# Performance work log

Hardware: AMD Instinct MI355X
Metric: run time of the kernel (lower is better)

## Reference

```python
import jax, jax.numpy as jnp
import numpy as np

B_, C_, H_, W_ = 4, 512, 64, 64

def setup_inputs() -> dict:
    key = jax.random.key(0)
    kx, kb, kc, kd, kg = jax.random.split(key, 5)
    scale = 1.0 / np.sqrt(C_)
    x = jax.random.normal(kx, (B_, C_, H_, W_), dtype=jnp.float32)
    Wb = jax.random.normal(kb, (C_, C_), dtype=jnp.float32) * scale
    Wc = jax.random.normal(kc, (C_, C_), dtype=jnp.float32) * scale
    Wd = jax.random.normal(kd, (C_, C_), dtype=jnp.float32) * scale
    gamma = jax.random.normal(kg, (1,), dtype=jnp.float32) * 0.1
    return {"x": x, "Wb": Wb, "Wc": Wc, "Wd": Wd, "gamma": gamma}

def reference(x, Wb, Wc, Wd, gamma):
    b, c, h, w = x.shape
    n = h * w
    xf = x.reshape(b, c, n)                       # (b, c, N)
    # 1x1 convs (bias=False) == per-pixel channel matmuls
    Bm = jnp.einsum('oc,bcn->bon', Wb, xf)        # (b, c, N)
    Cm = jnp.einsum('oc,bcn->bon', Wc, xf)
    Dm = jnp.einsum('oc,bcn->bon', Wd, xf)
    # S = softmax(B^T C, axis=2): (b, N, N), no scaling (faithful to source)
    S = jax.nn.softmax(jnp.einsum('bcn,bcm->bnm', Bm, Cm), axis=-1)
    # attention_maps = D @ S^T : (b, c, N)
    att = jnp.einsum('bcm,bnm->bcn', Dm, S).reshape(b, c, h, w)
    return gamma * att + x
```

## Files before the change

### kernel.cpp

```cpp
#include <hip/hip_runtime.h>
#include <math.h>
#include <stdint.h>

#define CC 512
#define NN 4096
#define BB 4

typedef _Float16 f16;
typedef _Float16 f16x8 __attribute__((ext_vector_type(8)));
typedef _Float16 f16x4 __attribute__((ext_vector_type(4)));
typedef float f32x4 __attribute__((ext_vector_type(4)));

__device__ __forceinline__ void gload_lds16(const void* g, void* l) {
    __builtin_amdgcn_global_load_lds(
        (const __attribute__((address_space(1))) void*)g,
        (__attribute__((address_space(3))) void*)l, 16, 0, 0);
}

template<int ROWS>
__device__ __forceinline__ void stage_tile(const f16* __restrict__ g, int stride_e,
                                           f16* lds, int wid, int lane) {
    constexpr int ITERS = ROWS * 8 / 64 / 4;
    #pragma unroll
    for (int it = 0; it < ITERS; ++it) {
        int flatbase = (wid * ITERS + it) * 64;
        f16* dst = lds + flatbase * 8;
        int flat = flatbase + lane;
        int r = flat >> 3, c = flat & 7;
        const f16* src = g + (size_t)r * stride_e + ((c ^ (r & 7)) << 3);
        gload_lds16(src, dst);
    }
}

__device__ __forceinline__ f16x8 frag_ld(const f16* lds, int r, int ch) {
    return *(const f16x8*)(lds + r * 64 + ((ch ^ (r & 7)) << 3));
}

#define MFMA16(a, b, c) __builtin_amdgcn_mfma_f32_16x16x32_f16((a), (b), (c), 0, 0, 0)

__device__ __forceinline__ f32x4 redmax16(f32x4 v) {
    #pragma unroll
    for (int off = 1; off < 16; off <<= 1) {
        f32x4 o;
        #pragma unroll
        for (int q = 0; q < 4; ++q) o[q] = __shfl_xor(v[q], off);
        #pragma unroll
        for (int q = 0; q < 4; ++q) v[q] = fmaxf(v[q], o[q]);
    }
    return v;
}
__device__ __forceinline__ f32x4 redsum16(f32x4 v) {
    #pragma unroll
    for (int off = 1; off < 16; off <<= 1) {
        f32x4 o;
        #pragma unroll
        for (int q = 0; q < 4; ++q) o[q] = __shfl_xor(v[q], off);
        #pragma unroll
        for (int q = 0; q < 4; ++q) v[q] += o[q];
    }
    return v;
}

__global__ __launch_bounds__(256) void wcvt_k(const float* __restrict__ Wb,
                                              const float* __restrict__ Wc,
                                              const float* __restrict__ Wd,
                                              f16* __restrict__ W16) {
    int i = blockIdx.x * 256 + threadIdx.x;
    int idx = i * 4;
    int m = idx >> 18;
    int off = idx & 262143;
    const float* src = (m == 0) ? Wb : (m == 1) ? Wc : Wd;
    f32x4 v = *(const f32x4*)(src + off);
    f16x4 h = { (f16)v[0], (f16)v[1], (f16)v[2], (f16)v[3] };
    *(f16x4*)(W16 + idx) = h;
}

__global__ __launch_bounds__(256) void proj_k(const float* __restrict__ x,
                                              const f16* __restrict__ W16,
                                              f16* __restrict__ Bt, f16* __restrict__ Ct,
                                              f16* __restrict__ Dm) {
    const int wsel = blockIdx.z % 3;
    const int b = blockIdx.z / 3;
    const f16* __restrict__ W = W16 + (size_t)wsel * CC * CC;
    const float* __restrict__ X = x + (size_t)b * CC * NN;
    const size_t p16 = (size_t)CC * NN;
    const int o0 = blockIdx.y * 128, n0 = blockIdx.x * 128;

    __shared__ __align__(16) char smraw[34816];
    f16* As = (f16*)smraw;
    f16* Bs = As + 128 * 64;
    f16* T  = (f16*)smraw;

    const int t = threadIdx.x;
    const int wid = t >> 6, lane = t & 63;
    const int wr = wid >> 1, wc = wid & 1;

    f32x4 acc[4][4] = {};
    const int cg = t & 7;
    const int n4 = ((t >> 3) & 31) * 4;

    for (int kc = 0; kc < CC; kc += 64) {
        __syncthreads();
        stage_tile<128>(W + (size_t)o0 * CC + kc, CC, As, wid, lane);
        f32x4 v[8];
        #pragma unroll
        for (int i = 0; i < 8; ++i)
            v[i] = *(const f32x4*)(X + (size_t)(kc + cg * 8 + i) * NN + n0 + n4);
        #pragma unroll
        for (int j = 0; j < 4; ++j) {
            f16x8 h = { (f16)v[0][j], (f16)v[1][j], (f16)v[2][j], (f16)v[3][j],
                        (f16)v[4][j], (f16)v[5][j], (f16)v[6][j], (f16)v[7][j] };
            int r = n4 + j;
            *(f16x8*)(Bs + r * 64 + ((cg ^ (r & 7)) << 3)) = h;
        }
        __syncthreads();
        #pragma unroll
        for (int ks = 0; ks < 2; ++ks) {
            int ch = ks * 4 + (lane >> 4);
            f16x8 a[4], bb[4];
            #pragma unroll
            for (int i = 0; i < 4; ++i) a[i]  = frag_ld(As, wr * 64 + i * 16 + (lane & 15), ch);
            #pragma unroll
            for (int j = 0; j < 4; ++j) bb[j] = frag_ld(Bs, wc * 64 + j * 16 + (lane & 15), ch);
            #pragma unroll
            for (int i = 0; i < 4; ++i)
                #pragma unroll
                for (int j = 0; j < 4; ++j)
                    acc[i][j] = MFMA16(a[i], bb[j], acc[i][j]);
        }
    }

    __syncthreads();
    if (wsel < 2) {
        #pragma unroll
        for (int i = 0; i < 4; ++i)
            #pragma unroll
            for (int j = 0; j < 4; ++j) {
                int n_l = wc * 64 + j * 16 + (lane & 15);
                int o_l = wr * 64 + i * 16 + (lane >> 4) * 4;
                f16x4 h = { (f16)acc[i][j][0], (f16)acc[i][j][1], (f16)acc[i][j][2], (f16)acc[i][j][3] };
                *(f16x4*)(T + n_l * 136 + o_l) = h;
            }
        __syncthreads();
        f16* __restrict__ dst = ((wsel == 0) ? Bt : Ct) + (size_t)b * p16;
        int n = t & 127;
        #pragma unroll
        for (int it = 0; it < 8; ++it) {
            int ch8 = (t >> 7) * 8 + it;
            f16x8 h = *(f16x8*)(T + n * 136 + ch8 * 8);
            *(f16x8*)(dst + (size_t)(n0 + n) * CC + o0 + ch8 * 8) = h;
        }
    } else {
        #pragma unroll
        for (int i = 0; i < 4; ++i)
            #pragma unroll
            for (int j = 0; j < 4; ++j) {
                int n_l = wc * 64 + j * 16 + (lane & 15);
                #pragma unroll
                for (int q = 0; q < 4; ++q) {
                    int o_l = wr * 64 + i * 16 + (lane >> 4) * 4 + q;
                    T[o_l * 136 + n_l] = (f16)acc[i][j][q];
                }
            }
        __syncthreads();
        f16* __restrict__ dst = Dm + (size_t)b * p16;
        int o = t & 127;
        #pragma unroll
        for (int it = 0; it < 8; ++it) {
            int ch8 = (t >> 7) * 8 + it;
            f16x8 h = *(f16x8*)(T + o * 136 + ch8 * 8);
            *(f16x8*)(dst + (size_t)(o0 + o) * NN + n0 + ch8 * 8) = h;
        }
    }
}

__global__ __launch_bounds__(512, 2) void flash_k(
    const float* __restrict__ x, const float* __restrict__ gamma_p,
    const f16* __restrict__ Bt, const f16* __restrict__ Ct,
    const f16* __restrict__ Dm, float* __restrict__ out)
{
    __shared__ __align__(16) char sm[140288];
    f16* CtS = (f16*)sm;
    f16* DtS = (f16*)(sm + 65536);
    f16* PS  = (f16*)(sm + 131072);
    float* mxp = (float*)(sm + 139264);
    float* lp  = (float*)(sm + 139776);

    const int bx = blockIdx.x;
    const int j8 = bx & 7;
    const int b = j8 >> 1;
    const int n0 = ((bx >> 3) + (j8 & 1) * 32) * 64;

    const size_t p16 = (size_t)CC * NN;
    const f16* __restrict__ Btb = Bt + (size_t)b * p16;
    const f16* __restrict__ Ctb = Ct + (size_t)b * p16;
    const f16* __restrict__ Dmb = Dm + (size_t)b * p16;

    const int t = threadIdx.x;
    const int wid = t >> 6, lane = t & 63;
    const int wr = wid >> 1, w1 = wid & 1;
    const int l15 = lane & 15, g = lane >> 4;

    f16x8 Q[16];
    {
        const f16* qrow = Btb + (size_t)(n0 + wr * 16 + l15) * CC + g * 8;
        #pragma unroll
        for (int s = 0; s < 16; ++s) Q[s] = *(const f16x8*)(qrow + s * 32);
    }

    f32x4 O[16];
    #pragma unroll
    for (int i = 0; i < 16; ++i) O[i] = (f32x4)(0.f);
    f32x4 m_run = (f32x4)(-INFINITY);
    f32x4 l_run = (f32x4)(0.f);

    for (int m0 = 0; m0 < NN; m0 += 64) {
        __syncthreads();
        #pragma unroll
        for (int it = 0; it < 8; ++it) {
            int r = wid * 8 + it;
            f16* dst = CtS + r * 512;
            const f16* src = Ctb + (size_t)(m0 + r) * CC + ((lane ^ (r & 7)) << 3);
            gload_lds16(src, dst);
        }
        #pragma unroll
        for (int it = 0; it < 8; ++it) {
            int flatbase = (wid * 8 + it) * 64;
            f16* dst = DtS + flatbase * 8;
            int flat = flatbase + lane;
            int r = flat >> 3, c = flat & 7;
            const f16* src = Dmb + (size_t)r * NN + m0 + ((c ^ (r & 7)) << 3);
            gload_lds16(src, dst);
        }
        __syncthreads();

        f32x4 S0 = (f32x4)(0.f), S1 = (f32x4)(0.f);
        #pragma unroll
        for (int s = 0; s < 16; ++s) {
            int ch = s * 4 + g;
            int mr0 = w1 * 32 + l15;
            int mr1 = mr0 + 16;
            f16x8 b0 = *(const f16x8*)(CtS + mr0 * 512 + (((ch ^ (mr0 & 7)) & 63) << 3));
            f16x8 b1 = *(const f16x8*)(CtS + mr1 * 512 + (((ch ^ (mr1 & 7)) & 63) << 3));
            S0 = MFMA16(Q[s], b0, S0);
            S1 = MFMA16(Q[s], b1, S1);
        }
        f32x4 tm;
        #pragma unroll
        for (int q = 0; q < 4; ++q) tm[q] = fmaxf(S0[q], S1[q]);
        tm = redmax16(tm);
        if (l15 == 0) *(f32x4*)(mxp + w1 * 64 + wr * 16 + g * 4) = tm;
        __syncthreads();
        f32x4 t0 = *(const f32x4*)(mxp + wr * 16 + g * 4);
        f32x4 t1 = *(const f32x4*)(mxp + 64 + wr * 16 + g * 4);
        f32x4 mnew, scl, p0, p1, ps;
        #pragma unroll
        for (int q = 0; q < 4; ++q) {
            mnew[q] = fmaxf(m_run[q], fmaxf(t0[q], t1[q]));
            scl[q] = __expf(m_run[q] - mnew[q]);
            p0[q] = __expf(S0[q] - mnew[q]);
            p1[q] = __expf(S1[q] - mnew[q]);
            ps[q] = p0[q] + p1[q];
        }
        m_run = mnew;
        ps = redsum16(ps);
        if (l15 == 0) *(f32x4*)(lp + w1 * 64 + wr * 16 + g * 4) = ps;
        #pragma unroll
        for (int q = 0; q < 4; ++q) {
            int row = wr * 16 + g * 4 + q;
            int c0 = w1 * 32 + l15;
            int c1 = c0 + 16;
            PS[row * 64 + ((((c0 >> 3) ^ (row & 7)) << 3) | (c0 & 7))] = (f16)p0[q];
            PS[row * 64 + ((((c1 >> 3) ^ (row & 7)) << 3) | (c1 & 7))] = (f16)p1[q];
        }
        __syncthreads();
        f32x4 lp0 = *(const f32x4*)(lp + wr * 16 + g * 4);
        f32x4 lp1 = *(const f32x4*)(lp + 64 + wr * 16 + g * 4);
        #pragma unroll
        for (int q = 0; q < 4; ++q) l_run[q] = l_run[q] * scl[q] + lp0[q] + lp1[q];
        #pragma unroll
        for (int i = 0; i < 16; ++i)
            #pragma unroll
            for (int q = 0; q < 4; ++q) O[i][q] *= scl[q];
        int prow = wr * 16 + l15;
        f16x8 pa0 = *(const f16x8*)(PS + prow * 64 + (((g ^ (prow & 7)) & 7) << 3));
        f16x8 pa1 = *(const f16x8*)(PS + prow * 64 + ((((4 + g) ^ (prow & 7)) & 7) << 3));
        #pragma unroll
        for (int jj = 0; jj < 16; ++jj) {
            int crow = w1 * 256 + jj * 16 + l15;
            f16x8 d0 = *(const f16x8*)(DtS + crow * 64 + (((g ^ (crow & 7)) & 7) << 3));
            f16x8 d1 = *(const f16x8*)(DtS + crow * 64 + ((((4 + g) ^ (crow & 7)) & 7) << 3));
            O[jj] = MFMA16(pa0, d0, O[jj]);
            O[jj] = MFMA16(pa1, d1, O[jj]);
        }
    }

    __syncthreads();
    const float gam = gamma_p[0];
    f32x4 inv;
    #pragma unroll
    for (int q = 0; q < 4; ++q) inv[q] = gam / l_run[q];
    float* T = (float*)sm;
    #pragma unroll
    for (int jj = 0; jj < 16; ++jj) {
        int crow = w1 * 256 + jj * 16 + l15;
        f32x4 v;
        #pragma unroll
        for (int q = 0; q < 4; ++q) v[q] = O[jj][q] * inv[q];
        *(f32x4*)(T + crow * 68 + wr * 16 + g * 4) = v;
    }
    __syncthreads();
    const float* __restrict__ xb = x + (size_t)b * CC * NN;
    float* __restrict__ ob = out + (size_t)b * CC * NN;
    #pragma unroll
    for (int it = 0; it < 16; ++it) {
        int c = (t >> 4) + it * 32;
        int n4 = (t & 15) * 4;
        f32x4 v = *(const f32x4*)(T + c * 68 + n4);
        f32x4 xv = *(const f32x4*)(xb + (size_t)c * NN + n0 + n4);
        #pragma unroll
        for (int q = 0; q < 4; ++q) v[q] += xv[q];
        *(f32x4*)(ob + (size_t)c * NN + n0 + n4) = v;
    }
}

extern "C" void kernel_launch(void* const* d_in, const int* in_sizes, int n_in,
                              void* d_out, int out_size, void* d_ws, size_t ws_size,
                              hipStream_t stream) {
    const float* x  = (const float*)d_in[0];
    const float* Wb = (const float*)d_in[1];
    const float* Wc = (const float*)d_in[2];
    const float* Wd = (const float*)d_in[3];
    const float* gm = (const float*)d_in[4];
    float* out = (float*)d_out;
    char* ws = (char*)d_ws;

    f16* W16 = (f16*)(ws);
    f16* Bt  = (f16*)(ws + 1572864);
    f16* Ct  = (f16*)(ws + 1572864 + 16777216);
    f16* Dm  = (f16*)(ws + 1572864 + 2 * 16777216);

    wcvt_k<<<dim3(768), 256, 0, stream>>>(Wb, Wc, Wd, W16);
    proj_k<<<dim3(32, 4, 12), 256, 0, stream>>>(x, W16, Bt, Ct, Dm);
    flash_k<<<dim3(256), 512, 0, stream>>>(x, gm, Bt, Ct, Dm, out);
}
```

Baseline: 385.5 us.

## Remap waves to 2x4 grid so each wave reuses LDS fragments across two row tiles

The eight waves move from a 4x2 layout (16 query rows, 32 keys, 256 output channels each) to a 2x4 layout (32 query rows, 16 keys, 128 output channels each). Each C and D fragment read from LDS now feeds two MFMAs, one per query row tile, which roughly halves LDS read traffic per MFMA in both the QK^T and PV phases. The cost is more Q registers per wave (32 fragments instead of 16), a cross-wave max/sum reduction over four partials instead of two, and a larger LDS footprint. s_setprio hints are also placed around the MFMA loops.

```diff
diff --git a/kernel.cpp b/kernel.cpp
--- a/kernel.cpp
+++ b/kernel.cpp
@@ -179,12 +179,12 @@
     const f16* __restrict__ Bt, const f16* __restrict__ Ct,
     const f16* __restrict__ Dm, float* __restrict__ out)
 {
-    __shared__ __align__(16) char sm[140288];
+    __shared__ __align__(16) char sm[141312];
     f16* CtS = (f16*)sm;
     f16* DtS = (f16*)(sm + 65536);
     f16* PS  = (f16*)(sm + 131072);
     float* mxp = (float*)(sm + 139264);
-    float* lp  = (float*)(sm + 139776);
+    float* lp  = (float*)(sm + 140288);
 
     const int bx = blockIdx.x;
     const int j8 = bx & 7;
@@ -198,21 +198,25 @@
 
     const int t = threadIdx.x;
     const int wid = t >> 6, lane = t & 63;
-    const int wr = wid >> 1, w1 = wid & 1;
+    const int a = wid >> 2, mj = wid & 3;
     const int l15 = lane & 15, g = lane >> 4;
-
-    f16x8 Q[16];
-    {
-        const f16* qrow = Btb + (size_t)(n0 + wr * 16 + l15) * CC + g * 8;
-        #pragma unroll
-        for (int s = 0; s < 16; ++s) Q[s] = *(const f16x8*)(qrow + s * 32);
-    }
-
-    f32x4 O[16];
-    #pragma unroll
-    for (int i = 0; i < 16; ++i) O[i] = (f32x4)(0.f);
-    f32x4 m_run = (f32x4)(-INFINITY);
-    f32x4 l_run = (f32x4)(0.f);
+    const int nb = a * 32 + g * 4;
+
+    f16x8 Q[2][16];
+    #pragma unroll
+    for (int f = 0; f < 2; ++f) {
+        const f16* qrow = Btb + (size_t)(n0 + a * 32 + f * 16 + l15) * CC + g * 8;
+        #pragma unroll
+        for (int s = 0; s < 16; ++s) Q[f][s] = *(const f16x8*)(qrow + s * 32);
+    }
+
+    f32x4 O[2][8];
+    #pragma unroll
+    for (int f = 0; f < 2; ++f)
+        #pragma unroll
+        for (int j = 0; j < 8; ++j) O[f][j] = (f32x4)(0.f);
+    f32x4 m_run[2] = { (f32x4)(-INFINITY), (f32x4)(-INFINITY) };
+    f32x4 l_run[2] = { (f32x4)(0.f), (f32x4)(0.f) };
 
     for (int m0 = 0; m0 < NN; m0 += 64) {
         __syncthreads();
@@ -235,80 +239,115 @@
         __syncthreads();
 
         f32x4 S0 = (f32x4)(0.f), S1 = (f32x4)(0.f);
+        const int mr = mj * 16 + l15;
+        __builtin_amdgcn_s_setprio(1);
         #pragma unroll
         for (int s = 0; s < 16; ++s) {
-            int ch = s * 4 + g;
-            int mr0 = w1 * 32 + l15;
-            int mr1 = mr0 + 16;
-            f16x8 b0 = *(const f16x8*)(CtS + mr0 * 512 + (((ch ^ (mr0 & 7)) & 63) << 3));
-            f16x8 b1 = *(const f16x8*)(CtS + mr1 * 512 + (((ch ^ (mr1 & 7)) & 63) << 3));
-            S0 = MFMA16(Q[s], b0, S0);
-            S1 = MFMA16(Q[s], b1, S1);
-        }
-        f32x4 tm;
-        #pragma unroll
-        for (int q = 0; q < 4; ++q) tm[q] = fmaxf(S0[q], S1[q]);
-        tm = redmax16(tm);
-        if (l15 == 0) *(f32x4*)(mxp + w1 * 64 + wr * 16 + g * 4) = tm;
-        __syncthreads();
-        f32x4 t0 = *(const f32x4*)(mxp + wr * 16 + g * 4);
-        f32x4 t1 = *(const f32x4*)(mxp + 64 + wr * 16 + g * 4);
-        f32x4 mnew, scl, p0, p1, ps;
+            f16x8 bfrag = *(const f16x8*)(CtS + mr * 512 + ((((s * 4 + g) ^ (mr & 7)) & 63) << 3));
+            S0 = MFMA16(Q[0][s], bfrag, S0);
+            S1 = MFMA16(Q[1][s], bfrag, S1);
+        }
+        __builtin_amdgcn_s_setprio(0);
+        f32x4 tm0 = redmax16(S0);
+        f32x4 tm1 = redmax16(S1);
+        if (l15 == 0) {
+            *(f32x4*)(mxp + mj * 64 + nb) = tm0;
+            *(f32x4*)(mxp + mj * 64 + nb + 16) = tm1;
+        }
+        __syncthreads();
+        f32x4 mnew[2], scl[2], p0, p1;
+        #pragma unroll
+        for (int f = 0; f < 2; ++f) {
+            f32x4 c0 = *(const f32x4*)(mxp + 0 * 64 + nb + f * 16);
+            f32x4 c1 = *(const f32x4*)(mxp + 1 * 64 + nb + f * 16);
+            f32x4 c2 = *(const f32x4*)(mxp + 2 * 64 + nb + f * 16);
+            f32x4 c3 = *(const f32x4*)(mxp + 3 * 64 + nb + f * 16);
+            #pragma unroll
+            for (int q = 0; q < 4; ++q) {
+                mnew[f][q] = fmaxf(m_run[f][q],
+                                   fmaxf(fmaxf(c0[q], c1[q]), fmaxf(c2[q], c3[q])));
+                scl[f][q] = __expf(m_run[f][q] - mnew[f][q]);
+            }
+            m_run[f] = mnew[f];
+        }
         #pragma unroll
         for (int q = 0; q < 4; ++q) {
-            mnew[q] = fmaxf(m_run[q], fmaxf(t0[q], t1[q]));
-            scl[q] = __expf(m_run[q] - mnew[q]);
-            p0[q] = __expf(S0[q] - mnew[q]);
-            p1[q] = __expf(S1[q] - mnew[q]);
-            ps[q] = p0[q] + p1[q];
-        }
-        m_run = mnew;
-        ps = redsum16(ps);
-        if (l15 == 0) *(f32x4*)(lp + w1 * 64 + wr * 16 + g * 4) = ps;
-        #pragma unroll
-        for (int q = 0; q < 4; ++q) {
-            int row = wr * 16 + g * 4 + q;
-            int c0 = w1 * 32 + l15;
-            int c1 = c0 + 16;
-            PS[row * 64 + ((((c0 >> 3) ^ (row & 7)) << 3) | (c0 & 7))] = (f16)p0[q];
-            PS[row * 64 + ((((c1 >> 3) ^ (row & 7)) << 3) | (c1 & 7))] = (f16)p1[q];
-        }
-        __syncthreads();
-        f32x4 lp0 = *(const f32x4*)(lp + wr * 16 + g * 4);
-        f32x4 lp1 = *(const f32x4*)(lp + 64 + wr * 16 + g * 4);
-        #pragma unroll
-        for (int q = 0; q < 4; ++q) l_run[q] = l_run[q] * scl[q] + lp0[q] + lp1[q];
-        #pragma unroll
-        for (int i = 0; i < 16; ++i)
-            #pragma unroll
-            for (int q = 0; q < 4; ++q) O[i][q] *= scl[q];
-        int prow = wr * 16 + l15;
-        f16x8 pa0 = *(const f16x8*)(PS + prow * 64 + (((g ^ (prow & 7)) & 7) << 3));
-        f16x8 pa1 = *(const f16x8*)(PS + prow * 64 + ((((4 + g) ^ (prow & 7)) & 7) << 3));
-        #pragma unroll
-        for (int jj = 0; jj < 16; ++jj) {
-            int crow = w1 * 256 + jj * 16 + l15;
-            f16x8 d0 = *(const f16x8*)(DtS + crow * 64 + (((g ^ (crow & 7)) & 7) << 3));
-            f16x8 d1 = *(const f16x8*)(DtS + crow * 64 + ((((4 + g) ^ (crow & 7)) & 7) << 3));
-            O[jj] = MFMA16(pa0, d0, O[jj]);
-            O[jj] = MFMA16(pa1, d1, O[jj]);
+            p0[q] = __expf(S0[q] - mnew[0][q]);
+            p1[q] = __expf(S1[q] - mnew[1][q]);
+        }
+        f32x4 ps0 = redsum16(p0);
+        f32x4 ps1 = redsum16(p1);
+        if (l15 == 0) {
+            *(f32x4*)(lp + mj * 64 + nb) = ps0;
+            *(f32x4*)(lp + mj * 64 + nb + 16) = ps1;
+        }
+        {
+            const int mcol = mj * 16 + l15;
+            #pragma unroll
+            for (int q = 0; q < 4; ++q) {
+                int r0 = nb + q;
+                int r1 = nb + 16 + q;
+                PS[r0 * 64 + ((((mcol >> 3) ^ (r0 & 7)) << 3) | (mcol & 7))] = (f16)p0[q];
+                PS[r1 * 64 + ((((mcol >> 3) ^ (r1 & 7)) << 3) | (mcol & 7))] = (f16)p1[q];
+            }
+        }
+        __syncthreads();
+        #pragma unroll
+        for (int f = 0; f < 2; ++f) {
+            f32x4 s0 = *(const f32x4*)(lp + 0 * 64 + nb + f * 16);
+            f32x4 s1 = *(const f32x4*)(lp + 1 * 64 + nb + f * 16);
+            f32x4 s2 = *(const f32x4*)(lp + 2 * 64 + nb + f * 16);
+            f32x4 s3 = *(const f32x4*)(lp + 3 * 64 + nb + f * 16);
+            #pragma unroll
+            for (int q = 0; q < 4; ++q)
+                l_run[f][q] = l_run[f][q] * scl[f][q] + s0[q] + s1[q] + s2[q] + s3[q];
+        }
+        #pragma unroll
+        for (int f = 0; f < 2; ++f)
+            #pragma unroll
+            for (int j = 0; j < 8; ++j)
+                #pragma unroll
+                for (int q = 0; q < 4; ++q)
+                    O[f][j][q] *= scl[f][q];
+        {
+            const int r0 = a * 32 + l15, r1 = r0 + 16;
+            f16x8 pa00 = *(const f16x8*)(PS + r0 * 64 + (((g ^ (r0 & 7)) & 7) << 3));
+            f16x8 pa01 = *(const f16x8*)(PS + r0 * 64 + ((((4 + g) ^ (r0 & 7)) & 7) << 3));
+            f16x8 pa10 = *(const f16x8*)(PS + r1 * 64 + (((g ^ (r1 & 7)) & 7) << 3));
+            f16x8 pa11 = *(const f16x8*)(PS + r1 * 64 + ((((4 + g) ^ (r1 & 7)) & 7) << 3));
+            __builtin_amdgcn_s_setprio(1);
+            #pragma unroll
+            for (int cf = 0; cf < 8; ++cf) {
+                int crow = mj * 128 + cf * 16 + l15;
+                f16x8 d0 = *(const f16x8*)(DtS + crow * 64 + (((g ^ (crow & 7)) & 7) << 3));
+                f16x8 d1 = *(const f16x8*)(DtS + crow * 64 + ((((4 + g) ^ (crow & 7)) & 7) << 3));
+                O[0][cf] = MFMA16(pa00, d0, O[0][cf]);
+                O[0][cf] = MFMA16(pa01, d1, O[0][cf]);
+                O[1][cf] = MFMA16(pa10, d0, O[1][cf]);
+                O[1][cf] = MFMA16(pa11, d1, O[1][cf]);
+            }
+            __builtin_amdgcn_s_setprio(0);
         }
     }
 
     __syncthreads();
     const float gam = gamma_p[0];
-    f32x4 inv;
-    #pragma unroll
-    for (int q = 0; q < 4; ++q) inv[q] = gam / l_run[q];
+    f32x4 inv[2];
+    #pragma unroll
+    for (int f = 0; f < 2; ++f)
+        #pragma unroll
+        for (int q = 0; q < 4; ++q) inv[f][q] = gam / l_run[f][q];
     float* T = (float*)sm;
     #pragma unroll
-    for (int jj = 0; jj < 16; ++jj) {
-        int crow = w1 * 256 + jj * 16 + l15;
-        f32x4 v;
-        #pragma unroll
-        for (int q = 0; q < 4; ++q) v[q] = O[jj][q] * inv[q];
-        *(f32x4*)(T + crow * 68 + wr * 16 + g * 4) = v;
-    }
+    for (int f = 0; f < 2; ++f)
+        #pragma unroll
+        for (int cf = 0; cf < 8; ++cf) {
+            int crow = mj * 128 + cf * 16 + l15;
+            f32x4 v;
+            #pragma unroll
+            for (int q = 0; q < 4; ++q) v[q] = O[f][cf][q] * inv[f][q];
+            *(f32x4*)(T + crow * 68 + nb + f * 16) = v;
+        }
     __syncthreads();
     const float* __restrict__ xb = x + (size_t)b * CC * NN;
     float* __restrict__ ob = out + (size_t)b * CC * NN;
```

New measurement: 844.0 us. +118.9%, slower.
